# Optimization experiments

Hardware: AMD Instinct MI355X
Metric: run time of the kernel (lower is better)

Reference implementation:

```python
import jax, jax.numpy as jnp
import numpy as np

EPS = 1e-15
MAX_TANH_ARG = 1.0 - 1e-5  # clamp for artanh domain, standard in Poincare-ball libs


def logmap0(x):
    # Poincare ball, c=1: logmap0(x) = artanh(||x||) * x / ||x||
    norm = jnp.linalg.norm(x, axis=-1, keepdims=True)
    norm_c = jnp.clip(norm, EPS, MAX_TANH_ARG)
    scale = jnp.arctanh(norm_c) / jnp.maximum(norm, EPS)
    return scale * x


def expmap0(v):
    # Poincare ball, c=1: expmap0(v) = tanh(||v||) * v / ||v||
    norm = jnp.linalg.norm(v, axis=-1, keepdims=True)
    scale = jnp.tanh(norm) / jnp.maximum(norm, EPS)
    return scale * v


def setup_inputs() -> dict:
    key = jax.random.key(0)
    k1, k2, k3, k4 = jax.random.split(key, 4)
    N, E, D_IN, D_OUT = 50000, 600000, 128, 128
    # points loosely inside/near the ball; logmap0 clamps the norm anyway
    x = jax.random.uniform(k1, (N, D_IN), dtype=jnp.float32)
    edge_index = jax.random.randint(k2, (2, E), 0, N, dtype=jnp.int32)
    W = jax.random.normal(k3, (D_OUT, D_IN), dtype=jnp.float32) / np.sqrt(D_IN)
    b = jax.random.normal(k4, (D_OUT,), dtype=jnp.float32) * 0.01
    return {"x": x, "edge_index": edge_index, "W": W, "b": b}


def reference(x, edge_index, W, b):
    num_nodes = x.shape[0]
    src, dst = edge_index[0], edge_index[1]

    x_tangent = logmap0(x)                       # [N, D_in]
    h = x_tangent @ W.T + b                      # [N, D_out]

    # symmetric degree count: each edge adds 1 to dst and 1 to src
    ones = jnp.ones(src.shape[0], dtype=jnp.float32)
    deg = (jax.ops.segment_sum(ones, dst, num_segments=num_nodes)
           + jax.ops.segment_sum(ones, src, num_segments=num_nodes))
    deg = jnp.maximum(deg, 1.0)
    dinv = deg ** -0.5                           # [N]

    # fused gather-scale-scatter across ALL feature dims at once
    msg = h[src] * (dinv[src] * dinv[dst])[:, None]   # [E, D_out]
    out = jax.ops.segment_sum(msg, dst, num_segments=num_nodes)  # [N, D_out]

    return expmap0(out)
```

## Files before the change

### kernel.cpp

```cpp
#include <hip/hip_runtime.h>
#include <math.h>

#define D 128
#define CAP 48
#define NS 32
#define HWPAD 12512
#define HB (NS * 2)

typedef __attribute__((ext_vector_type(8))) short short8;
typedef __attribute__((ext_vector_type(4))) float f32x4;

__device__ inline unsigned short f2bf(float f) {
  unsigned int u = __float_as_uint(f);
  u = (u + 0x7FFFu + ((u >> 16) & 1u)) >> 16;
  return (unsigned short)u;
}
__device__ inline float bf2f(unsigned int us) {
  return __uint_as_float(us << 16);
}

__global__ __launch_bounds__(256) void k_prep(
    const float* __restrict__ W, const int* __restrict__ src,
    const int* __restrict__ dst, unsigned int* __restrict__ e32,
    unsigned short* __restrict__ Wbf, unsigned int* __restrict__ cursor,
    unsigned int* __restrict__ part, int N, int E, int fancy) {
  const int t = threadIdx.x;
  const int bid = blockIdx.x;

  if (bid < HB) {
    if (!fancy) return;
    __shared__ unsigned int lh[HWPAD];
    const int s = bid >> 1, hf = bid & 1;
    const int W16 = (N + 1) >> 1;
    const int HW = (W16 + 1) >> 1;
    const unsigned int baseW = (unsigned)(hf * HW);
    for (int i = t; i < HWPAD; i += 256) lh[i] = 0u;
    __syncthreads();
    const int e0 = (int)((long long)s * E / NS);
    const int e1 = (int)((long long)(s + 1) * E / NS);
    for (int e = e0 + t; e < e1; e += 256) {
      int d_ = dst[e], s_ = src[e];
      unsigned int wd = ((unsigned)d_ >> 1) - baseW;
      if (wd < (unsigned)HW) atomicAdd(&lh[wd], 1u << ((d_ & 1) << 4));
      unsigned int ws = ((unsigned)s_ >> 1) - baseW;
      if (ws < (unsigned)HW) atomicAdd(&lh[ws], 1u << ((s_ & 1) << 4));
    }
    __syncthreads();
    uint4* po = (uint4*)(part + (size_t)bid * HWPAD);
    const uint4* li = (const uint4*)lh;
    for (int i = t; i < HWPAD / 4; i += 256) po[i] = li[i];
    return;
  }

  int g = (bid - HB) * 256 + t;
  if (g < N) cursor[g] = 0u;
  if (fancy) {
    int e = g * 4;
    if (e + 3 < E) {
      int4 s4 = *(const int4*)(src + e);
      int4 d4 = *(const int4*)(dst + e);
      uint4 p;
      p.x = ((unsigned)d4.x << 16) | (unsigned)s4.x;
      p.y = ((unsigned)d4.y << 16) | (unsigned)s4.y;
      p.z = ((unsigned)d4.z << 16) | (unsigned)s4.z;
      p.w = ((unsigned)d4.w << 16) | (unsigned)s4.w;
      *(uint4*)(e32 + e) = p;
    } else if (e < E) {
      for (int k = e; k < E; ++k)
        e32[k] = ((unsigned)dst[k] << 16) | (unsigned)src[k];
    }
  }
  int i = g * 4;
  if (i < D * D) {
    float4 wv = *(const float4*)(W + i);
    int r = i >> 7, c = i & 127;
    int idx = ((c >> 3) << 10) + (r << 3) + (c & 7);
    *(ushort4*)(&Wbf[idx]) =
        make_ushort4(f2bf(wv.x), f2bf(wv.y), f2bf(wv.z), f2bf(wv.w));
  }
}

__global__ __launch_bounds__(256) void k_fused(
    const float* __restrict__ x, const unsigned short* __restrict__ Wbf,
    const float* __restrict__ bvec, const int* __restrict__ src,
    const int* __restrict__ dst, const unsigned int* __restrict__ e32,
    unsigned int* __restrict__ cursor, int* __restrict__ ebuf,
    float* __restrict__ dinv, const unsigned int* __restrict__ part,
    unsigned short* __restrict__ h, int N, int E, int RB, int ET, int fancy) {
  const int t = threadIdx.x;
  const int bid = blockIdx.x;

  if (bid < RB) {
    const int W16 = (N + 1) >> 1;
    const int HW = (W16 + 1) >> 1;
    int wd = bid * 256 + t;
    if (wd < W16) {
      int hf = (wd >= HW);
      int lw = wd - hf * HW;
      const unsigned int* p = part + (size_t)hf * HWPAD + lw;
      unsigned int sum = 0;
#pragma unroll
      for (int s = 0; s < NS; ++s) sum += p[(size_t)s * 2 * HWPAD];
      int n0 = wd * 2;
      float d0 = rsqrtf(fmaxf((float)(sum & 0xFFFFu), 1.0f));
      float d1 = rsqrtf(fmaxf((float)(sum >> 16), 1.0f));
      if (n0 + 1 < N)
        *(float2*)(dinv + n0) = make_float2(d0, d1);
      else if (n0 < N)
        dinv[n0] = d0;
    }
    return;
  }

  const int fb = bid - RB;
  const int w = t >> 6;
  const int l = t & 63;

  if (w >= 2) {
    const int base = fb * 128 + (t - 128);
    if (fancy) {
      unsigned int ev[3];
      bool v[3];
#pragma unroll
      for (int i = 0; i < 3; ++i) {
        int e = base + i * ET;
        v[i] = (e < E);
        ev[i] = v[i] ? e32[e] : 0u;
      }
      unsigned int pos[3] = {0xFFFFFFFFu, 0xFFFFFFFFu, 0xFFFFFFFFu};
#pragma unroll
      for (int i = 0; i < 3; ++i)
        if (v[i]) pos[i] = atomicAdd(&cursor[ev[i] >> 16], 1u);
#pragma unroll
      for (int i = 0; i < 3; ++i)
        if (pos[i] < CAP)
          ebuf[(size_t)(ev[i] >> 16) * CAP + pos[i]] = (int)(ev[i] & 0xFFFFu);
      for (int e = base + 3 * ET; e < E; e += ET) {
        unsigned int v_ = e32[e];
        unsigned int p = atomicAdd(&cursor[v_ >> 16], 1u);
        if (p < CAP) ebuf[(size_t)(v_ >> 16) * CAP + p] = (int)(v_ & 0xFFFFu);
      }
    } else {
      for (int e = base; e < E; e += ET) {
        int d_ = dst[e], s_ = src[e];
        unsigned int p = atomicAdd(&cursor[d_], 1u) & 0xFFFFu;
        if (p < CAP) ebuf[(size_t)d_ * CAP + p] = s_;
        atomicAdd(&cursor[s_], 0x10000u);
      }
    }
    return;
  }

  const int lc = l & 15;
  const int q = l >> 4;
  const int r0 = fb * 32;
  const int grow = r0 + w * 16 + lc;
  const bool ok = grow < N;
  const float* xp = x + (size_t)grow * D + q * 8;

  short8 a[4];
  float ss = 0.0f;
#pragma unroll
  for (int kk = 0; kk < 4; ++kk) {
    float4 u = ok ? *(const float4*)(xp + kk * 32) : make_float4(0, 0, 0, 0);
    float4 v = ok ? *(const float4*)(xp + kk * 32 + 4) : make_float4(0, 0, 0, 0);
    ss += u.x * u.x + u.y * u.y + u.z * u.z + u.w * u.w;
    ss += v.x * v.x + v.y * v.y + v.z * v.z + v.w * v.w;
    short8 af;
    af[0] = (short)f2bf(u.x); af[1] = (short)f2bf(u.y);
    af[2] = (short)f2bf(u.z); af[3] = (short)f2bf(u.w);
    af[4] = (short)f2bf(v.x); af[5] = (short)f2bf(v.y);
    af[6] = (short)f2bf(v.z); af[7] = (short)f2bf(v.w);
    a[kk] = af;
  }
  ss += __shfl_xor(ss, 16, 64);
  ss += __shfl_xor(ss, 32, 64);
  float nrm = sqrtf(ss);
  float nc = fminf(fmaxf(nrm, 1e-15f), 1.0f - 1e-5f);
  float rs = atanhf(nc) / fmaxf(nrm, 1e-15f);

  f32x4 acc[8];
#pragma unroll
  for (int nt = 0; nt < 8; ++nt) acc[nt] = (f32x4){0.f, 0.f, 0.f, 0.f};

#pragma unroll
  for (int kk = 0; kk < 4; ++kk) {
#pragma unroll
    for (int nt = 0; nt < 8; ++nt) {
      short8 bf =
          *(const short8*)(Wbf + ((kk * 4 + q) << 10) + ((nt * 16 + lc) << 3));
      acc[nt] = __builtin_amdgcn_mfma_f32_16x16x32_bf16(a[kk], bf, acc[nt], 0, 0, 0);
    }
  }

  float rsl[4];
#pragma unroll
  for (int i = 0; i < 4; ++i) rsl[i] = __shfl(rs, q * 4 + i, 64);

#pragma unroll
  for (int nt = 0; nt < 8; ++nt) {
    int j = nt * 16 + lc;
    float bj = bvec[j];
#pragma unroll
    for (int i = 0; i < 4; ++i) {
      int gr = r0 + w * 16 + q * 4 + i;
      if (gr < N) h[(size_t)gr * D + j] = f2bf(rsl[i] * acc[nt][i] + bj);
    }
  }
}

__global__ __launch_bounds__(256) void k_gather(
    const unsigned short* __restrict__ h, const int* __restrict__ ebuf,
    const unsigned int* __restrict__ cursor, const float* __restrict__ dinv,
    float* __restrict__ out, int N, int fancy) {
  int gid = blockIdx.x * 256 + threadIdx.x;
  int r = gid >> 5;
  int sub = threadIdx.x & 31;
  if (r >= N) return;

  unsigned int cr = cursor[r];
  int cnt = fancy ? (int)cr : (int)(cr & 0xFFFFu);
  if (cnt > CAP) cnt = CAP;
  float di_d = fancy ? dinv[r]
                     : rsqrtf(fmaxf((float)((cr & 0xFFFFu) + (cr >> 16)), 1.0f));
  const int* eb = ebuf + (size_t)r * CAP;

  int c1 = cnt < 32 ? cnt : 32;
  int s_a = (sub < c1) ? eb[sub] : 0;
  float dv_a = 0.0f;
  if (sub < c1) {
    if (fancy) dv_a = dinv[s_a];
    else {
      unsigned int vs = cursor[s_a];
      dv_a = rsqrtf(fmaxf((float)((vs & 0xFFFFu) + (vs >> 16)), 1.0f));
    }
  }
  int s_b = (sub + 32 < cnt) ? eb[32 + sub] : 0;
  float dv_b = 0.0f;
  if (sub + 32 < cnt) {
    if (fancy) dv_b = dinv[s_b];
    else {
      unsigned int vs = cursor[s_b];
      dv_b = rsqrtf(fmaxf((float)((vs & 0xFFFFu) + (vs >> 16)), 1.0f));
    }
  }

  float a0 = 0.f, a1 = 0.f, a2 = 0.f, a3 = 0.f;
  for (int i = 0; i < c1; i += 8) {
    uint2 pv[8];
    float wj[8];
#pragma unroll
    for (int j = 0; j < 8; ++j) {
      int s = __shfl(s_a, i + j, 32);
      wj[j] = __shfl(dv_a, i + j, 32);
      pv[j] = *(const uint2*)(h + (size_t)s * D + sub * 4);
    }
#pragma unroll
    for (int j = 0; j < 8; ++j) {
      a0 += wj[j] * bf2f(pv[j].x & 0xFFFFu);
      a1 += wj[j] * bf2f(pv[j].x >> 16);
      a2 += wj[j] * bf2f(pv[j].y & 0xFFFFu);
      a3 += wj[j] * bf2f(pv[j].y >> 16);
    }
  }
  for (int i = 0; i < cnt - 32; i += 8) {
    uint2 pv[8];
    float wj[8];
#pragma unroll
    for (int j = 0; j < 8; ++j) {
      int s = __shfl(s_b, i + j, 32);
      wj[j] = __shfl(dv_b, i + j, 32);
      pv[j] = *(const uint2*)(h + (size_t)s * D + sub * 4);
    }
#pragma unroll
    for (int j = 0; j < 8; ++j) {
      a0 += wj[j] * bf2f(pv[j].x & 0xFFFFu);
      a1 += wj[j] * bf2f(pv[j].x >> 16);
      a2 += wj[j] * bf2f(pv[j].y & 0xFFFFu);
      a3 += wj[j] * bf2f(pv[j].y >> 16);
    }
  }

  a0 *= di_d; a1 *= di_d; a2 *= di_d; a3 *= di_d;

  float sN = a0 * a0 + a1 * a1 + a2 * a2 + a3 * a3;
#pragma unroll
  for (int off = 16; off > 0; off >>= 1) sN += __shfl_down(sN, off, 32);
  sN = __shfl(sN, 0, 32);
  float n = sqrtf(sN);
  float sc = tanhf(n) / fmaxf(n, 1e-15f);

  float4* op = (float4*)(out + (size_t)r * D);
  op[sub] = make_float4(a0 * sc, a1 * sc, a2 * sc, a3 * sc);
}

extern "C" void kernel_launch(void* const* d_in, const int* in_sizes, int n_in,
                              void* d_out, int out_size, void* d_ws, size_t ws_size,
                              hipStream_t stream) {
  const float* x = (const float*)d_in[0];
  const int* ei = (const int*)d_in[1];
  const float* W = (const float*)d_in[2];
  const float* b = (const float*)d_in[3];
  float* out = (float*)d_out;

  const int N = in_sizes[0] / D;
  const int E = in_sizes[1] / 2;
  const int* src = ei;
  const int* dst = ei + E;

  size_t o_ebuf = ((size_t)N * D * 2 + 63) & ~(size_t)63;
  size_t o_cur = (o_ebuf + (size_t)N * CAP * 4 + 63) & ~(size_t)63;
  size_t o_dinv = (o_cur + (size_t)N * 4 + 63) & ~(size_t)63;
  size_t o_wbf = (o_dinv + (size_t)N * 4 + 63) & ~(size_t)63;
  size_t o_e32 = (o_wbf + 32768 + 63) & ~(size_t)63;
  size_t o_part = (o_e32 + (size_t)E * 4 + 63) & ~(size_t)63;
  size_t need = o_part + (size_t)HB * HWPAD * 4;

  unsigned short* h = (unsigned short*)d_ws;
  int* ebuf = (int*)((char*)d_ws + o_ebuf);
  unsigned int* cursor = (unsigned int*)((char*)d_ws + o_cur);
  float* dinv = (float*)((char*)d_ws + o_dinv);
  unsigned short* Wbf = (unsigned short*)((char*)d_ws + o_wbf);
  unsigned int* e32 = (unsigned int*)((char*)d_ws + o_e32);
  unsigned int* part = (unsigned int*)((char*)d_ws + o_part);

  const int W16 = (N + 1) >> 1;
  const int HW = (W16 + 1) >> 1;
  const int fancy = (HW <= HWPAD) && (N <= 65535) && (ws_size >= need);

  int PBn = (N + 255) / 256;
  int PBe = ((E + 3) / 4 + 255) / 256;
  int PB = PBn > 16 ? PBn : 16;
  if (fancy && PBe > PB) PB = PBe;
  k_prep<<<HB + PB, 256, 0, stream>>>(W, src, dst, e32, Wbf, cursor, part, N, E,
                                      fancy);

  const int RB = fancy ? (W16 + 255) / 256 : 0;
  const int NBG = (N + 31) / 32;
  const int ET = NBG * 128;
  k_fused<<<RB + NBG, 256, 0, stream>>>(x, Wbf, b, src, dst, e32, cursor, ebuf,
                                        dinv, part, h, N, E, RB, ET, fancy);
  k_gather<<<(int)(((long long)N * 32 + 255) / 256), 256, 0, stream>>>(
      h, ebuf, cursor, dinv, out, N, fancy);
}
```

Baseline: 165.1 us.

## Replace global-atomic edge bucketing with prefix-histogram slot assignment and widen gather

The degree histogram is split into separate dst and src partial histograms. The bucketing blocks seed an LDS histogram with the prefix sum of earlier slices' dst counts and take each edge's slot from a shared-memory atomic, replacing global atomics on the cursor array. Each node's in-count is stored in a new cntv array. The linear-transform blocks now use all four waves to cover 64 rows. The gather kernel uses 16 lanes per row with 16-byte bf16 loads and 8 accumulators per lane. The cost is that every bucketing block re-reads up to 31 partial histograms to build its prefix, which adds substantial L2 traffic.

```diff
diff --git a/kernel.cpp b/kernel.cpp
--- a/kernel.cpp
+++ b/kernel.cpp
@@ -5,7 +5,8 @@
 #define CAP 48
 #define NS 32
 #define HWPAD 12512
-#define HB (NS * 2)
+#define HBH (NS * 2)
+#define HB (HBH * 2)
 
 typedef __attribute__((ext_vector_type(8))) short short8;
 typedef __attribute__((ext_vector_type(4))) float f32x4;
@@ -30,7 +31,9 @@
   if (bid < HB) {
     if (!fancy) return;
     __shared__ unsigned int lh[HWPAD];
-    const int s = bid >> 1, hf = bid & 1;
+    const int kind = bid >> 6;
+    const int sb = bid & 63;
+    const int s = sb >> 1, hf = sb & 1;
     const int W16 = (N + 1) >> 1;
     const int HW = (W16 + 1) >> 1;
     const unsigned int baseW = (unsigned)(hf * HW);
@@ -38,15 +41,14 @@
     __syncthreads();
     const int e0 = (int)((long long)s * E / NS);
     const int e1 = (int)((long long)(s + 1) * E / NS);
+    const int* key = kind ? src : dst;
     for (int e = e0 + t; e < e1; e += 256) {
-      int d_ = dst[e], s_ = src[e];
-      unsigned int wd = ((unsigned)d_ >> 1) - baseW;
-      if (wd < (unsigned)HW) atomicAdd(&lh[wd], 1u << ((d_ & 1) << 4));
-      unsigned int ws = ((unsigned)s_ >> 1) - baseW;
-      if (ws < (unsigned)HW) atomicAdd(&lh[ws], 1u << ((s_ & 1) << 4));
+      int n = key[e];
+      unsigned int wk = ((unsigned)n >> 1) - baseW;
+      if (wk < (unsigned)HW) atomicAdd(&lh[wk], 1u << ((n & 1) << 4));
     }
     __syncthreads();
-    uint4* po = (uint4*)(part + (size_t)bid * HWPAD);
+    uint4* po = (uint4*)(part + (size_t)(kind * HBH + sb) * HWPAD);
     const uint4* li = (const uint4*)lh;
     for (int i = t; i < HWPAD / 4; i += 256) po[i] = li[i];
     return;
@@ -80,13 +82,15 @@
   }
 }
 
-__global__ __launch_bounds__(256) void k_fused(
+__global__ __launch_bounds__(256) void k_main(
     const float* __restrict__ x, const unsigned short* __restrict__ Wbf,
     const float* __restrict__ bvec, const int* __restrict__ src,
     const int* __restrict__ dst, const unsigned int* __restrict__ e32,
     unsigned int* __restrict__ cursor, int* __restrict__ ebuf,
-    float* __restrict__ dinv, const unsigned int* __restrict__ part,
-    unsigned short* __restrict__ h, int N, int E, int RB, int ET, int fancy) {
+    float* __restrict__ dinv, unsigned int* __restrict__ cntv,
+    const unsigned int* __restrict__ part, unsigned short* __restrict__ h,
+    int N, int E, int RB, int BKB, int fancy) {
+  __shared__ unsigned int lh[HWPAD];
   const int t = threadIdx.x;
   const int bid = blockIdx.x;
 
@@ -97,51 +101,59 @@
     if (wd < W16) {
       int hf = (wd >= HW);
       int lw = wd - hf * HW;
-      const unsigned int* p = part + (size_t)hf * HWPAD + lw;
-      unsigned int sum = 0;
-#pragma unroll
-      for (int s = 0; s < NS; ++s) sum += p[(size_t)s * 2 * HWPAD];
+      unsigned int si = 0, so = 0;
+#pragma unroll
+      for (int s = 0; s < NS; ++s) {
+        si += part[(size_t)(s * 2 + hf) * HWPAD + lw];
+        so += part[(size_t)(HBH + s * 2 + hf) * HWPAD + lw];
+      }
       int n0 = wd * 2;
-      float d0 = rsqrtf(fmaxf((float)(sum & 0xFFFFu), 1.0f));
-      float d1 = rsqrtf(fmaxf((float)(sum >> 16), 1.0f));
-      if (n0 + 1 < N)
-        *(float2*)(dinv + n0) = make_float2(d0, d1);
-      else if (n0 < N)
-        dinv[n0] = d0;
+      unsigned int in0 = si & 0xFFFFu, in1 = si >> 16;
+      float d0 = rsqrtf(fmaxf((float)(in0 + (so & 0xFFFFu)), 1.0f));
+      float d1 = rsqrtf(fmaxf((float)(in1 + (so >> 16)), 1.0f));
+      cntv[n0] = in0;
+      dinv[n0] = d0;
+      if (n0 + 1 < N) {
+        cntv[n0 + 1] = in1;
+        dinv[n0 + 1] = d1;
+      }
     }
     return;
   }
 
-  const int fb = bid - RB;
-  const int w = t >> 6;
-  const int l = t & 63;
-
-  if (w >= 2) {
-    const int base = fb * 128 + (t - 128);
+  if (bid < RB + BKB) {
+    const int sb = bid - RB;
     if (fancy) {
-      unsigned int ev[3];
-      bool v[3];
-#pragma unroll
-      for (int i = 0; i < 3; ++i) {
-        int e = base + i * ET;
-        v[i] = (e < E);
-        ev[i] = v[i] ? e32[e] : 0u;
-      }
-      unsigned int pos[3] = {0xFFFFFFFFu, 0xFFFFFFFFu, 0xFFFFFFFFu};
-#pragma unroll
-      for (int i = 0; i < 3; ++i)
-        if (v[i]) pos[i] = atomicAdd(&cursor[ev[i] >> 16], 1u);
-#pragma unroll
-      for (int i = 0; i < 3; ++i)
-        if (pos[i] < CAP)
-          ebuf[(size_t)(ev[i] >> 16) * CAP + pos[i]] = (int)(ev[i] & 0xFFFFu);
-      for (int e = base + 3 * ET; e < E; e += ET) {
-        unsigned int v_ = e32[e];
-        unsigned int p = atomicAdd(&cursor[v_ >> 16], 1u);
-        if (p < CAP) ebuf[(size_t)(v_ >> 16) * CAP + p] = (int)(v_ & 0xFFFFu);
+      const int s = sb >> 1, hf = sb & 1;
+      const int W16 = (N + 1) >> 1;
+      const int HW = (W16 + 1) >> 1;
+      const unsigned int baseW = (unsigned)(hf * HW);
+      for (int i = t; i < HWPAD / 4; i += 256) {
+        uint4 a = make_uint4(0, 0, 0, 0);
+        for (int sp = 0; sp < s; ++sp) {
+          uint4 v = *(const uint4*)(part + (size_t)(sp * 2 + hf) * HWPAD + i * 4);
+          a.x += v.x; a.y += v.y; a.z += v.z; a.w += v.w;
+        }
+        ((uint4*)lh)[i] = a;
+      }
+      __syncthreads();
+      const int e0 = (int)((long long)s * E / NS);
+      const int e1 = (int)((long long)(s + 1) * E / NS);
+      for (int e = e0 + t; e < e1; e += 256) {
+        unsigned int v = e32[e];
+        int d_ = (int)(v >> 16);
+        unsigned int wk = ((unsigned)d_ >> 1) - baseW;
+        if (wk < (unsigned)HW) {
+          int sh = (d_ & 1) << 4;
+          unsigned int old = atomicAdd(&lh[wk], 1u << sh);
+          unsigned int slot = (old >> sh) & 0xFFFFu;
+          if (slot < CAP) ebuf[(size_t)d_ * CAP + slot] = (int)(v & 0xFFFFu);
+        }
       }
     } else {
-      for (int e = base; e < E; e += ET) {
+      const int e0 = (int)((long long)sb * E / BKB);
+      const int e1 = (int)((long long)(sb + 1) * E / BKB);
+      for (int e = e0 + t; e < e1; e += 256) {
         int d_ = dst[e], s_ = src[e];
         unsigned int p = atomicAdd(&cursor[d_], 1u) & 0xFFFFu;
         if (p < CAP) ebuf[(size_t)d_ * CAP + p] = s_;
@@ -151,9 +163,12 @@
     return;
   }
 
+  const int gb = bid - RB - BKB;
+  const int w = t >> 6;
+  const int l = t & 63;
   const int lc = l & 15;
   const int q = l >> 4;
-  const int r0 = fb * 32;
+  const int r0 = gb * 64;
   const int grow = r0 + w * 16 + lc;
   const bool ok = grow < N;
   const float* xp = x + (size_t)grow * D + q * 8;
@@ -212,86 +227,90 @@
 __global__ __launch_bounds__(256) void k_gather(
     const unsigned short* __restrict__ h, const int* __restrict__ ebuf,
     const unsigned int* __restrict__ cursor, const float* __restrict__ dinv,
-    float* __restrict__ out, int N, int fancy) {
+    const unsigned int* __restrict__ cntv, float* __restrict__ out, int N,
+    int fancy) {
   int gid = blockIdx.x * 256 + threadIdx.x;
-  int r = gid >> 5;
-  int sub = threadIdx.x & 31;
+  int r = gid >> 4;
+  int sub = threadIdx.x & 15;
   if (r >= N) return;
 
-  unsigned int cr = cursor[r];
-  int cnt = fancy ? (int)cr : (int)(cr & 0xFFFFu);
+  int cnt;
+  float di_d;
+  if (fancy) {
+    cnt = (int)cntv[r];
+    di_d = dinv[r];
+  } else {
+    unsigned int cr = cursor[r];
+    cnt = (int)(cr & 0xFFFFu);
+    di_d = rsqrtf(fmaxf((float)((cr & 0xFFFFu) + (cr >> 16)), 1.0f));
+  }
   if (cnt > CAP) cnt = CAP;
-  float di_d = fancy ? dinv[r]
-                     : rsqrtf(fmaxf((float)((cr & 0xFFFFu) + (cr >> 16)), 1.0f));
   const int* eb = ebuf + (size_t)r * CAP;
 
-  int c1 = cnt < 32 ? cnt : 32;
-  int s_a = (sub < c1) ? eb[sub] : 0;
-  float dv_a = 0.0f;
-  if (sub < c1) {
-    if (fancy) dv_a = dinv[s_a];
-    else {
-      unsigned int vs = cursor[s_a];
-      dv_a = rsqrtf(fmaxf((float)((vs & 0xFFFFu) + (vs >> 16)), 1.0f));
-    }
-  }
-  int s_b = (sub + 32 < cnt) ? eb[32 + sub] : 0;
-  float dv_b = 0.0f;
-  if (sub + 32 < cnt) {
-    if (fancy) dv_b = dinv[s_b];
-    else {
-      unsigned int vs = cursor[s_b];
-      dv_b = rsqrtf(fmaxf((float)((vs & 0xFFFFu) + (vs >> 16)), 1.0f));
-    }
-  }
+#define GETDV(sidx)                                                      \
+  (fancy ? dinv[sidx] : ({                                               \
+    unsigned int vs_ = cursor[sidx];                                     \
+    rsqrtf(fmaxf((float)((vs_ & 0xFFFFu) + (vs_ >> 16)), 1.0f));         \
+  }))
+
+  int s0 = (sub < cnt) ? eb[sub] : 0;
+  float dv0 = (sub < cnt) ? GETDV(s0) : 0.0f;
+  int s1 = (16 + sub < cnt) ? eb[16 + sub] : 0;
+  float dv1 = (16 + sub < cnt) ? GETDV(s1) : 0.0f;
+  int s2 = (32 + sub < cnt) ? eb[32 + sub] : 0;
+  float dv2 = (32 + sub < cnt) ? GETDV(s2) : 0.0f;
+#undef GETDV
 
   float a0 = 0.f, a1 = 0.f, a2 = 0.f, a3 = 0.f;
-  for (int i = 0; i < c1; i += 8) {
-    uint2 pv[8];
-    float wj[8];
-#pragma unroll
-    for (int j = 0; j < 8; ++j) {
-      int s = __shfl(s_a, i + j, 32);
-      wj[j] = __shfl(dv_a, i + j, 32);
-      pv[j] = *(const uint2*)(h + (size_t)s * D + sub * 4);
-    }
-#pragma unroll
-    for (int j = 0; j < 8; ++j) {
-      a0 += wj[j] * bf2f(pv[j].x & 0xFFFFu);
-      a1 += wj[j] * bf2f(pv[j].x >> 16);
-      a2 += wj[j] * bf2f(pv[j].y & 0xFFFFu);
-      a3 += wj[j] * bf2f(pv[j].y >> 16);
-    }
-  }
-  for (int i = 0; i < cnt - 32; i += 8) {
-    uint2 pv[8];
-    float wj[8];
-#pragma unroll
-    for (int j = 0; j < 8; ++j) {
-      int s = __shfl(s_b, i + j, 32);
-      wj[j] = __shfl(dv_b, i + j, 32);
-      pv[j] = *(const uint2*)(h + (size_t)s * D + sub * 4);
-    }
-#pragma unroll
-    for (int j = 0; j < 8; ++j) {
-      a0 += wj[j] * bf2f(pv[j].x & 0xFFFFu);
-      a1 += wj[j] * bf2f(pv[j].x >> 16);
-      a2 += wj[j] * bf2f(pv[j].y & 0xFFFFu);
-      a3 += wj[j] * bf2f(pv[j].y >> 16);
-    }
-  }
+  float a4 = 0.f, a5 = 0.f, a6 = 0.f, a7 = 0.f;
+
+#define CHUNK8(SV, DV, CNT2)                                              \
+  for (int i = 0; i < (CNT2); i += 8) {                                   \
+    uint4 pv[8];                                                          \
+    float wj[8];                                                          \
+    _Pragma("unroll") for (int j = 0; j < 8; ++j) {                       \
+      int s = __shfl(SV, i + j, 16);                                      \
+      wj[j] = __shfl(DV, i + j, 16);                                      \
+      pv[j] = *(const uint4*)(h + (size_t)s * D + sub * 8);               \
+    }                                                                     \
+    _Pragma("unroll") for (int j = 0; j < 8; ++j) {                       \
+      a0 += wj[j] * bf2f(pv[j].x & 0xFFFFu);                              \
+      a1 += wj[j] * bf2f(pv[j].x >> 16);                                  \
+      a2 += wj[j] * bf2f(pv[j].y & 0xFFFFu);                              \
+      a3 += wj[j] * bf2f(pv[j].y >> 16);                                  \
+      a4 += wj[j] * bf2f(pv[j].z & 0xFFFFu);                              \
+      a5 += wj[j] * bf2f(pv[j].z >> 16);                                  \
+      a6 += wj[j] * bf2f(pv[j].w & 0xFFFFu);                              \
+      a7 += wj[j] * bf2f(pv[j].w >> 16);                                  \
+    }                                                                     \
+  }
+
+  int c1 = cnt < 16 ? cnt : 16;
+  CHUNK8(s0, dv0, c1);
+  if (cnt > 16) {
+    int c2 = (cnt < 32 ? cnt : 32) - 16;
+    CHUNK8(s1, dv1, c2);
+  }
+  if (cnt > 32) {
+    int c3 = cnt - 32;
+    CHUNK8(s2, dv2, c3);
+  }
+#undef CHUNK8
 
   a0 *= di_d; a1 *= di_d; a2 *= di_d; a3 *= di_d;
-
-  float sN = a0 * a0 + a1 * a1 + a2 * a2 + a3 * a3;
-#pragma unroll
-  for (int off = 16; off > 0; off >>= 1) sN += __shfl_down(sN, off, 32);
-  sN = __shfl(sN, 0, 32);
+  a4 *= di_d; a5 *= di_d; a6 *= di_d; a7 *= di_d;
+
+  float sN = a0 * a0 + a1 * a1 + a2 * a2 + a3 * a3 + a4 * a4 + a5 * a5 +
+             a6 * a6 + a7 * a7;
+#pragma unroll
+  for (int off = 8; off > 0; off >>= 1) sN += __shfl_down(sN, off, 16);
+  sN = __shfl(sN, 0, 16);
   float n = sqrtf(sN);
   float sc = tanhf(n) / fmaxf(n, 1e-15f);
 
-  float4* op = (float4*)(out + (size_t)r * D);
-  op[sub] = make_float4(a0 * sc, a1 * sc, a2 * sc, a3 * sc);
+  float* op = out + (size_t)r * D + sub * 8;
+  *(float4*)op = make_float4(a0 * sc, a1 * sc, a2 * sc, a3 * sc);
+  *(float4*)(op + 4) = make_float4(a4 * sc, a5 * sc, a6 * sc, a7 * sc);
 }
 
 extern "C" void kernel_launch(void* const* d_in, const int* in_sizes, int n_in,
@@ -311,7 +330,8 @@
   size_t o_ebuf = ((size_t)N * D * 2 + 63) & ~(size_t)63;
   size_t o_cur = (o_ebuf + (size_t)N * CAP * 4 + 63) & ~(size_t)63;
   size_t o_dinv = (o_cur + (size_t)N * 4 + 63) & ~(size_t)63;
-  size_t o_wbf = (o_dinv + (size_t)N * 4 + 63) & ~(size_t)63;
+  size_t o_cnt = (o_dinv + (size_t)N * 4 + 63) & ~(size_t)63;
+  size_t o_wbf = (o_cnt + (size_t)N * 4 + 63) & ~(size_t)63;
   size_t o_e32 = (o_wbf + 32768 + 63) & ~(size_t)63;
   size_t o_part = (o_e32 + (size_t)E * 4 + 63) & ~(size_t)63;
   size_t need = o_part + (size_t)HB * HWPAD * 4;
@@ -320,6 +340,7 @@
   int* ebuf = (int*)((char*)d_ws + o_ebuf);
   unsigned int* cursor = (unsigned int*)((char*)d_ws + o_cur);
   float* dinv = (float*)((char*)d_ws + o_dinv);
+  unsigned int* cntv = (unsigned int*)((char*)d_ws + o_cnt);
   unsigned short* Wbf = (unsigned short*)((char*)d_ws + o_wbf);
   unsigned int* e32 = (unsigned int*)((char*)d_ws + o_e32);
   unsigned int* part = (unsigned int*)((char*)d_ws + o_part);
@@ -336,10 +357,11 @@
                                       fancy);
 
   const int RB = fancy ? (W16 + 255) / 256 : 0;
-  const int NBG = (N + 31) / 32;
-  const int ET = NBG * 128;
-  k_fused<<<RB + NBG, 256, 0, stream>>>(x, Wbf, b, src, dst, e32, cursor, ebuf,
-                                        dinv, part, h, N, E, RB, ET, fancy);
-  k_gather<<<(int)(((long long)N * 32 + 255) / 256), 256, 0, stream>>>(
-      h, ebuf, cursor, dinv, out, N, fancy);
-}
+  const int BKB = 64;
+  const int NBG = (N + 63) / 64;
+  k_main<<<RB + BKB + NBG, 256, 0, stream>>>(x, Wbf, b, src, dst, e32, cursor,
+                                             ebuf, dinv, cntv, part, h, N, E,
+                                             RB, BKB, fancy);
+  k_gather<<<(int)(((long long)N * 16 + 255) / 256), 256, 0, stream>>>(
+      h, ebuf, cursor, dinv, cntv, out, N, fancy);
+}
```

New measurement: 199.1 us. 20.6% more time.

## Replace global atomic edge bucketing with shared-histogram rank-based counting sort

Applied to the files above, without the earlier changes.

Edge bucketing by destination is now a counting sort. The histogram blocks record each edge's local rank from shared-memory atomics, and a separate reduce kernel computes per-slice prefix offsets, in-degree counts and dinv. Each edge is then placed at prefix+rank without global atomics. The GEMM blocks now cover 64 rows using all four waves. The cost is an extra launch, doubled histogram blocks, and extra rank/prefix buffers to write and read.

```diff
diff --git a/kernel.cpp b/kernel.cpp
--- a/kernel.cpp
+++ b/kernel.cpp
@@ -5,7 +5,9 @@
 #define CAP 48
 #define NS 32
 #define HWPAD 12512
-#define HB (NS * 2)
+#define HBH (NS * 2)
+#define HB (HBH * 2)
+#define BKB 64
 
 typedef __attribute__((ext_vector_type(8))) short short8;
 typedef __attribute__((ext_vector_type(4))) float f32x4;
@@ -23,14 +25,17 @@
     const float* __restrict__ W, const int* __restrict__ src,
     const int* __restrict__ dst, unsigned int* __restrict__ e32,
     unsigned short* __restrict__ Wbf, unsigned int* __restrict__ cursor,
-    unsigned int* __restrict__ part, int N, int E, int fancy) {
+    unsigned int* __restrict__ part, unsigned char* __restrict__ rank, int N,
+    int E, int fancy) {
   const int t = threadIdx.x;
   const int bid = blockIdx.x;
 
   if (bid < HB) {
     if (!fancy) return;
     __shared__ unsigned int lh[HWPAD];
-    const int s = bid >> 1, hf = bid & 1;
+    const int kind = bid >> 6;
+    const int sb = bid & 63;
+    const int s = sb >> 1, hf = sb & 1;
     const int W16 = (N + 1) >> 1;
     const int HW = (W16 + 1) >> 1;
     const unsigned int baseW = (unsigned)(hf * HW);
@@ -38,15 +43,26 @@
     __syncthreads();
     const int e0 = (int)((long long)s * E / NS);
     const int e1 = (int)((long long)(s + 1) * E / NS);
-    for (int e = e0 + t; e < e1; e += 256) {
-      int d_ = dst[e], s_ = src[e];
-      unsigned int wd = ((unsigned)d_ >> 1) - baseW;
-      if (wd < (unsigned)HW) atomicAdd(&lh[wd], 1u << ((d_ & 1) << 4));
-      unsigned int ws = ((unsigned)s_ >> 1) - baseW;
-      if (ws < (unsigned)HW) atomicAdd(&lh[ws], 1u << ((s_ & 1) << 4));
+    if (kind == 0) {
+      for (int e = e0 + t; e < e1; e += 256) {
+        int n = dst[e];
+        unsigned int wk = ((unsigned)n >> 1) - baseW;
+        if (wk < (unsigned)HW) {
+          int sh = (n & 1) << 4;
+          unsigned int old = atomicAdd(&lh[wk], 1u << sh);
+          unsigned int rk = (old >> sh) & 0xFFFFu;
+          rank[e] = (unsigned char)(rk > 255u ? 255u : rk);
+        }
+      }
+    } else {
+      for (int e = e0 + t; e < e1; e += 256) {
+        int n = src[e];
+        unsigned int wk = ((unsigned)n >> 1) - baseW;
+        if (wk < (unsigned)HW) atomicAdd(&lh[wk], 1u << ((n & 1) << 4));
+      }
     }
     __syncthreads();
-    uint4* po = (uint4*)(part + (size_t)bid * HWPAD);
+    uint4* po = (uint4*)(part + (size_t)(kind * HBH + sb) * HWPAD);
     const uint4* li = (const uint4*)lh;
     for (int i = t; i < HWPAD / 4; i += 256) po[i] = li[i];
     return;
@@ -80,68 +96,61 @@
   }
 }
 
-__global__ __launch_bounds__(256) void k_fused(
+__global__ __launch_bounds__(256) void k_reduce(
+    const unsigned int* __restrict__ part, float* __restrict__ dinv,
+    unsigned int* __restrict__ cntv, unsigned short* __restrict__ pre, int N) {
+  const int W16 = (N + 1) >> 1;
+  const int HW = (W16 + 1) >> 1;
+  int wd = blockIdx.x * 256 + threadIdx.x;
+  if (wd >= W16) return;
+  int hf = (wd >= HW);
+  int lw = wd - hf * HW;
+  int n0 = wd * 2;
+  unsigned int run = 0, so = 0;
+#pragma unroll
+  for (int s = 0; s < NS; ++s) {
+    unsigned short* pp = pre + (size_t)s * N + n0;
+    pp[0] = (unsigned short)(run & 0xFFFFu);
+    if (n0 + 1 < N) pp[1] = (unsigned short)(run >> 16);
+    run += part[(size_t)(s * 2 + hf) * HWPAD + lw];
+    so += part[(size_t)(HBH + s * 2 + hf) * HWPAD + lw];
+  }
+  unsigned int in0 = run & 0xFFFFu, in1 = run >> 16;
+  cntv[n0] = in0;
+  dinv[n0] = rsqrtf(fmaxf((float)(in0 + (so & 0xFFFFu)), 1.0f));
+  if (n0 + 1 < N) {
+    cntv[n0 + 1] = in1;
+    dinv[n0 + 1] = rsqrtf(fmaxf((float)(in1 + (so >> 16)), 1.0f));
+  }
+}
+
+__global__ __launch_bounds__(256) void k_main(
     const float* __restrict__ x, const unsigned short* __restrict__ Wbf,
     const float* __restrict__ bvec, const int* __restrict__ src,
     const int* __restrict__ dst, const unsigned int* __restrict__ e32,
     unsigned int* __restrict__ cursor, int* __restrict__ ebuf,
-    float* __restrict__ dinv, const unsigned int* __restrict__ part,
-    unsigned short* __restrict__ h, int N, int E, int RB, int ET, int fancy) {
+    const unsigned char* __restrict__ rank,
+    const unsigned short* __restrict__ pre, unsigned short* __restrict__ h,
+    int N, int E, int fancy) {
   const int t = threadIdx.x;
   const int bid = blockIdx.x;
 
-  if (bid < RB) {
-    const int W16 = (N + 1) >> 1;
-    const int HW = (W16 + 1) >> 1;
-    int wd = bid * 256 + t;
-    if (wd < W16) {
-      int hf = (wd >= HW);
-      int lw = wd - hf * HW;
-      const unsigned int* p = part + (size_t)hf * HWPAD + lw;
-      unsigned int sum = 0;
-#pragma unroll
-      for (int s = 0; s < NS; ++s) sum += p[(size_t)s * 2 * HWPAD];
-      int n0 = wd * 2;
-      float d0 = rsqrtf(fmaxf((float)(sum & 0xFFFFu), 1.0f));
-      float d1 = rsqrtf(fmaxf((float)(sum >> 16), 1.0f));
-      if (n0 + 1 < N)
-        *(float2*)(dinv + n0) = make_float2(d0, d1);
-      else if (n0 < N)
-        dinv[n0] = d0;
-    }
-    return;
-  }
-
-  const int fb = bid - RB;
-  const int w = t >> 6;
-  const int l = t & 63;
-
-  if (w >= 2) {
-    const int base = fb * 128 + (t - 128);
+  if (bid < BKB) {
     if (fancy) {
-      unsigned int ev[3];
-      bool v[3];
-#pragma unroll
-      for (int i = 0; i < 3; ++i) {
-        int e = base + i * ET;
-        v[i] = (e < E);
-        ev[i] = v[i] ? e32[e] : 0u;
-      }
-      unsigned int pos[3] = {0xFFFFFFFFu, 0xFFFFFFFFu, 0xFFFFFFFFu};
-#pragma unroll
-      for (int i = 0; i < 3; ++i)
-        if (v[i]) pos[i] = atomicAdd(&cursor[ev[i] >> 16], 1u);
-#pragma unroll
-      for (int i = 0; i < 3; ++i)
-        if (pos[i] < CAP)
-          ebuf[(size_t)(ev[i] >> 16) * CAP + pos[i]] = (int)(ev[i] & 0xFFFFu);
-      for (int e = base + 3 * ET; e < E; e += ET) {
-        unsigned int v_ = e32[e];
-        unsigned int p = atomicAdd(&cursor[v_ >> 16], 1u);
-        if (p < CAP) ebuf[(size_t)(v_ >> 16) * CAP + p] = (int)(v_ & 0xFFFFu);
+      const int s = bid >> 1;
+      const int e0 = (int)((long long)s * E / NS);
+      const int e1 = (int)((long long)(s + 1) * E / NS);
+      const unsigned short* ps = pre + (size_t)s * N;
+      for (int e = e0 + (bid & 1) * 256 + t; e < e1; e += 512) {
+        unsigned int v = e32[e];
+        int d_ = (int)(v >> 16);
+        unsigned int slot = (unsigned int)ps[d_] + (unsigned int)rank[e];
+        if (slot < CAP) ebuf[(size_t)d_ * CAP + slot] = (int)(v & 0xFFFFu);
       }
     } else {
-      for (int e = base; e < E; e += ET) {
+      const int e0 = (int)((long long)bid * E / BKB);
+      const int e1 = (int)((long long)(bid + 1) * E / BKB);
+      for (int e = e0 + t; e < e1; e += 256) {
         int d_ = dst[e], s_ = src[e];
         unsigned int p = atomicAdd(&cursor[d_], 1u) & 0xFFFFu;
         if (p < CAP) ebuf[(size_t)d_ * CAP + p] = s_;
@@ -151,9 +160,12 @@
     return;
   }
 
+  const int gb = bid - BKB;
+  const int w = t >> 6;
+  const int l = t & 63;
   const int lc = l & 15;
   const int q = l >> 4;
-  const int r0 = fb * 32;
+  const int r0 = gb * 64;
   const int grow = r0 + w * 16 + lc;
   const bool ok = grow < N;
   const float* xp = x + (size_t)grow * D + q * 8;
@@ -212,17 +224,24 @@
 __global__ __launch_bounds__(256) void k_gather(
     const unsigned short* __restrict__ h, const int* __restrict__ ebuf,
     const unsigned int* __restrict__ cursor, const float* __restrict__ dinv,
-    float* __restrict__ out, int N, int fancy) {
+    const unsigned int* __restrict__ cntv, float* __restrict__ out, int N,
+    int fancy) {
   int gid = blockIdx.x * 256 + threadIdx.x;
   int r = gid >> 5;
   int sub = threadIdx.x & 31;
   if (r >= N) return;
 
-  unsigned int cr = cursor[r];
-  int cnt = fancy ? (int)cr : (int)(cr & 0xFFFFu);
+  int cnt;
+  float di_d;
+  if (fancy) {
+    cnt = (int)cntv[r];
+    di_d = dinv[r];
+  } else {
+    unsigned int cr = cursor[r];
+    cnt = (int)(cr & 0xFFFFu);
+    di_d = rsqrtf(fmaxf((float)((cr & 0xFFFFu) + (cr >> 16)), 1.0f));
+  }
   if (cnt > CAP) cnt = CAP;
-  float di_d = fancy ? dinv[r]
-                     : rsqrtf(fmaxf((float)((cr & 0xFFFFu) + (cr >> 16)), 1.0f));
   const int* eb = ebuf + (size_t)r * CAP;
 
   int c1 = cnt < 32 ? cnt : 32;
@@ -311,18 +330,24 @@
   size_t o_ebuf = ((size_t)N * D * 2 + 63) & ~(size_t)63;
   size_t o_cur = (o_ebuf + (size_t)N * CAP * 4 + 63) & ~(size_t)63;
   size_t o_dinv = (o_cur + (size_t)N * 4 + 63) & ~(size_t)63;
-  size_t o_wbf = (o_dinv + (size_t)N * 4 + 63) & ~(size_t)63;
+  size_t o_cnt = (o_dinv + (size_t)N * 4 + 63) & ~(size_t)63;
+  size_t o_wbf = (o_cnt + (size_t)N * 4 + 63) & ~(size_t)63;
   size_t o_e32 = (o_wbf + 32768 + 63) & ~(size_t)63;
   size_t o_part = (o_e32 + (size_t)E * 4 + 63) & ~(size_t)63;
-  size_t need = o_part + (size_t)HB * HWPAD * 4;
+  size_t o_pre = (o_part + (size_t)HB * HWPAD * 4 + 63) & ~(size_t)63;
+  size_t o_rank = (o_pre + (size_t)NS * N * 2 + 63) & ~(size_t)63;
+  size_t need = o_rank + (size_t)E;
 
   unsigned short* h = (unsigned short*)d_ws;
   int* ebuf = (int*)((char*)d_ws + o_ebuf);
   unsigned int* cursor = (unsigned int*)((char*)d_ws + o_cur);
   float* dinv = (float*)((char*)d_ws + o_dinv);
+  unsigned int* cntv = (unsigned int*)((char*)d_ws + o_cnt);
   unsigned short* Wbf = (unsigned short*)((char*)d_ws + o_wbf);
   unsigned int* e32 = (unsigned int*)((char*)d_ws + o_e32);
   unsigned int* part = (unsigned int*)((char*)d_ws + o_part);
+  unsigned short* pre = (unsigned short*)((char*)d_ws + o_pre);
+  unsigned char* rank = (unsigned char*)((char*)d_ws + o_rank);
 
   const int W16 = (N + 1) >> 1;
   const int HW = (W16 + 1) >> 1;
@@ -332,14 +357,15 @@
   int PBe = ((E + 3) / 4 + 255) / 256;
   int PB = PBn > 16 ? PBn : 16;
   if (fancy && PBe > PB) PB = PBe;
-  k_prep<<<HB + PB, 256, 0, stream>>>(W, src, dst, e32, Wbf, cursor, part, N, E,
-                                      fancy);
-
-  const int RB = fancy ? (W16 + 255) / 256 : 0;
-  const int NBG = (N + 31) / 32;
-  const int ET = NBG * 128;
-  k_fused<<<RB + NBG, 256, 0, stream>>>(x, Wbf, b, src, dst, e32, cursor, ebuf,
-                                        dinv, part, h, N, E, RB, ET, fancy);
+  k_prep<<<HB + PB, 256, 0, stream>>>(W, src, dst, e32, Wbf, cursor, part, rank,
+                                      N, E, fancy);
+
+  if (fancy)
+    k_reduce<<<(W16 + 255) / 256, 256, 0, stream>>>(part, dinv, cntv, pre, N);
+
+  const int NBG = (N + 63) / 64;
+  k_main<<<BKB + NBG, 256, 0, stream>>>(x, Wbf, b, src, dst, e32, cursor, ebuf,
+                                        rank, pre, h, N, E, fancy);
   k_gather<<<(int)(((long long)N * 32 + 255) / 256), 256, 0, stream>>>(
-      h, ebuf, cursor, dinv, out, N, fancy);
-}
+      h, ebuf, cursor, dinv, cntv, out, N, fancy);
+}
```

Result: slower. 171.7 us (+4.0%).
